# Kernel optimization log

Hardware: AMD Instinct MI355X
Metric: run time of the kernel (lower is better)

The kernel has to match this reference:

```python
import jax, jax.numpy as jnp
import numpy as np

# Mamba2 hyperparameters (from init_kwargs + mamba_ssm defaults)
D_MODEL = 1024
D_STATE = 64
D_CONV = 4
EXPAND = 2
HEADDIM = 64                      # mamba_ssm default
D_INNER = EXPAND * D_MODEL        # 2048
NHEADS = D_INNER // HEADDIM       # 32
NGROUPS = 1
CONV_DIM = D_INNER + 2 * NGROUPS * D_STATE      # 2176
D_IN_PROJ = 2 * D_INNER + 2 * NGROUPS * D_STATE + NHEADS  # 4256
BATCH, SEQLEN = 4, 2048


def setup_inputs() -> dict:
    key = jax.random.key(0)
    ks = jax.random.split(key, 8)
    x = jax.random.normal(ks[0], (BATCH, SEQLEN, D_MODEL), dtype=jnp.float32)
    W_in = jax.random.normal(ks[1], (D_MODEL, D_IN_PROJ), dtype=jnp.float32) * 0.02
    conv_w = jax.random.normal(ks[2], (CONV_DIM, D_CONV), dtype=jnp.float32) * 0.2
    conv_b = jnp.zeros((CONV_DIM,), dtype=jnp.float32)
    # dt_bias = inverse-softplus of dt ~ U(1e-3, 0.1), as in mamba_ssm init
    dt = jnp.exp(jax.random.uniform(ks[3], (NHEADS,)) * (np.log(0.1) - np.log(1e-3)) + np.log(1e-3))
    dt_bias = dt + jnp.log(-jnp.expm1(-dt))
    A_log = jnp.log(jax.random.uniform(ks[4], (NHEADS,), minval=1.0, maxval=16.0))
    D = jnp.ones((NHEADS,), dtype=jnp.float32)
    norm_w = jnp.ones((D_INNER,), dtype=jnp.float32)
    W_out = jax.random.normal(ks[5], (D_INNER, D_MODEL), dtype=jnp.float32) * 0.02
    return {"x": x, "W_in": W_in, "conv_w": conv_w, "conv_b": conv_b,
            "dt_bias": dt_bias, "A_log": A_log, "D": D, "norm_w": norm_w, "W_out": W_out}


def _mamba2_forward(x, W_in, conv_w, conv_b, dt_bias, A_log, D, norm_w, W_out):
    Bsz, L, _ = x.shape
    zxbcdt = x @ W_in                                   # [B, L, D_IN_PROJ]
    z = zxbcdt[..., :D_INNER]                           # gate
    xBC = zxbcdt[..., D_INNER:D_INNER + CONV_DIM]
    dt = zxbcdt[..., D_INNER + CONV_DIM:]               # [B, L, H]
    dt = jax.nn.softplus(dt + dt_bias)

    # causal depthwise conv1d over time, kernel width D_CONV
    xp = jnp.pad(xBC, ((0, 0), (D_CONV - 1, 0), (0, 0)))
    xc = sum(xp[:, k:k + L, :] * conv_w[:, k] for k in range(D_CONV))
    xBC = jax.nn.silu(xc + conv_b)

    xh = xBC[..., :D_INNER].reshape(Bsz, L, NHEADS, HEADDIM)   # [B,L,H,P]
    Bm = xBC[..., D_INNER:D_INNER + D_STATE]                   # [B,L,N] (ngroups=1)
    Cm = xBC[..., D_INNER + D_STATE:]                          # [B,L,N]
    A = -jnp.exp(A_log)                                        # [H]

    # selective SSM scan: h_t = h_{t-1}*exp(dt_t*A) + dt_t * x_t (outer) B_t ; y_t = C_t . h_t
    def step(h, inp):
        dt_t, x_t, B_t, C_t = inp                 # [B,H],[B,H,P],[B,N],[B,N]
        dA = jnp.exp(dt_t * A)                    # [B,H]
        h = h * dA[..., None, None] + (dt_t[..., None] * x_t)[..., None] * B_t[:, None, None, :]
        y_t = jnp.einsum('bhpn,bn->bhp', h, C_t)
        return h, y_t

    h0 = jnp.zeros((Bsz, NHEADS, HEADDIM, D_STATE), dtype=x.dtype)
    inputs = (jnp.moveaxis(dt, 1, 0), jnp.moveaxis(xh, 1, 0),
              jnp.moveaxis(Bm, 1, 0), jnp.moveaxis(Cm, 1, 0))
    _, ys = jax.lax.scan(step, h0, inputs)                     # [L,B,H,P]
    y = jnp.moveaxis(ys, 0, 1) + xh * D[None, None, :, None]   # skip term D*x
    y = y.reshape(Bsz, L, D_INNER)

    # gated RMSNorm: norm(y * silu(z)) * weight
    y = y * jax.nn.silu(z)
    y = y * jax.lax.rsqrt(jnp.mean(y * y, axis=-1, keepdims=True) + 1e-5) * norm_w
    return y @ W_out


def reference(x, W_in, conv_w, conv_b, dt_bias, A_log, D, norm_w, W_out):
    return _mamba2_forward(x, W_in, conv_w, conv_b, dt_bias, A_log, D, norm_w, W_out)
```

## Files before the change

kernel.cpp:

```cpp
#include <hip/hip_runtime.h>
#include <hip/hip_bf16.h>

#define B_SZ   4
#define SEQ    2048
#define DM     1024
#define DIN    2048
#define DST    64
#define NH     32
#define HD     64
#define CONVD  2176
#define DPROJ  4256
#define NPAD1  4352
#define MROWS  (B_SZ*SEQ)
#define QC     64
#define NC     (SEQ/QC)

typedef __attribute__((ext_vector_type(8))) __bf16 bf16x8;
typedef __attribute__((ext_vector_type(4))) __bf16 bf16x4;
typedef __attribute__((ext_vector_type(4))) float  floatx4;

__device__ __forceinline__ int swz(int row, int col) {
    return row * 64 + ((((col >> 3) ^ (row & 7)) << 3) | (col & 7));
}
__device__ __forceinline__ float bfbits2f(unsigned short u) {
    return __uint_as_float(((unsigned int)u) << 16);
}
__device__ __forceinline__ unsigned short f2bfbits(float f) {
    union { __bf16 h; unsigned short u; } cv; cv.h = (__bf16)f; return cv.u;
}

__global__ __launch_bounds__(256) void dtw_prep_kernel(const float* __restrict__ W_in,
                                                       float* __restrict__ dtWc) {
    int idx = blockIdx.x * 256 + threadIdx.x;
    int k = idx >> 5, h = idx & 31;
    dtWc[idx] = W_in[(size_t)k * DPROJ + 2 * DIN + 2 * DST + h];
}

__global__ __launch_bounds__(256) void cvt_dt_kernel(const float* __restrict__ x,
                                                     const float* __restrict__ dtWc,
                                                     __bf16* __restrict__ xbf,
                                                     float* __restrict__ dtraw) {
    __shared__ float xs[4][DM];
    __shared__ float red[4][8][32];
    const int row0 = blockIdx.x * 4;
    const int tid = threadIdx.x;
    #pragma unroll
    for (int r = 0; r < 4; r++) {
        float4 v = ((const float4*)(x + (size_t)(row0 + r) * DM))[tid];
        bf16x4 o;
        o[0] = (__bf16)v.x; o[1] = (__bf16)v.y; o[2] = (__bf16)v.z; o[3] = (__bf16)v.w;
        *(bf16x4*)(xbf + (size_t)(row0 + r) * DM + tid * 4) = o;
        xs[r][tid * 4 + 0] = v.x; xs[r][tid * 4 + 1] = v.y;
        xs[r][tid * 4 + 2] = v.z; xs[r][tid * 4 + 3] = v.w;
    }
    __syncthreads();
    const int part = tid >> 5, h = tid & 31;
    const float* wb = dtWc + part * 128 * 32 + h;
    const int kb = part * 128;
    float s0 = 0.f, s1 = 0.f, s2 = 0.f, s3 = 0.f;
    for (int j = 0; j < 128; j++) {
        float w = wb[j * 32];
        s0 = fmaf(xs[0][kb + j], w, s0);
        s1 = fmaf(xs[1][kb + j], w, s1);
        s2 = fmaf(xs[2][kb + j], w, s2);
        s3 = fmaf(xs[3][kb + j], w, s3);
    }
    red[0][part][h] = s0; red[1][part][h] = s1;
    red[2][part][h] = s2; red[3][part][h] = s3;
    __syncthreads();
    if (tid < 128) {
        int r = tid >> 5, hh = tid & 31;
        float s = 0.f;
        #pragma unroll
        for (int p = 0; p < 8; p++) s += red[r][p][hh];
        dtraw[(size_t)(row0 + r) * NH + hh] = s;
    }
}

__global__ __launch_bounds__(256) void transpose_cvt_kernel(const float* __restrict__ src,
                                                            __bf16* __restrict__ dst,
                                                            int R, int C, int Crows) {
    __shared__ float tile[32][33];
    int r0 = blockIdx.x * 32, c0 = blockIdx.y * 32;
    int tx = threadIdx.x & 31, ty = threadIdx.x >> 5;
    #pragma unroll
    for (int i = 0; i < 4; i++) {
        int r = r0 + ty + i * 8, c = c0 + tx;
        float v = (r < R && c < C) ? src[(size_t)r * C + c] : 0.f;
        tile[ty + i * 8][tx] = v;
    }
    __syncthreads();
    #pragma unroll
    for (int i = 0; i < 4; i++) {
        int cc = c0 + ty + i * 8, rr = r0 + tx;
        if (cc < Crows && rr < R)
            dst[(size_t)cc * R + rr] = (__bf16)tile[tx][ty + i * 8];
    }
}

template<int STORE_BF16>
__global__ __launch_bounds__(256) void gemm_bt_kernel(const __bf16* __restrict__ A,
                                                      const __bf16* __restrict__ Bt,
                                                      float* __restrict__ Cf,
                                                      __bf16* __restrict__ Cb,
                                                      int M, int N, int K) {
    __shared__ __align__(16) __bf16 As[128][32];
    __shared__ __align__(16) __bf16 Bs[128][32];
    const int tid = threadIdx.x;
    const int m0 = blockIdx.x * 128, n0 = blockIdx.y * 128;
    const int wave = tid >> 6, lane = tid & 63;
    const int wm = (wave & 1) << 6, wn = (wave >> 1) << 6;
    const int lm = lane & 15, lq = lane >> 4;

    floatx4 acc[4][4] = {};

    for (int k0 = 0; k0 < K; k0 += 32) {
        #pragma unroll
        for (int r = 0; r < 2; r++) {
            int c = tid + (r << 8);
            int row = c >> 2, off = (c & 3) << 3;
            __builtin_amdgcn_global_load_lds(
                reinterpret_cast<const unsigned int*>(&A[(size_t)(m0 + row) * K + k0 + off]),
                reinterpret_cast<unsigned int*>(&As[0][0] + (size_t)c * 8), 16, 0, 0);
            __builtin_amdgcn_global_load_lds(
                reinterpret_cast<const unsigned int*>(&Bt[(size_t)(n0 + row) * K + k0 + off]),
                reinterpret_cast<unsigned int*>(&Bs[0][0] + (size_t)c * 8), 16, 0, 0);
        }
        __syncthreads();
        bf16x8 af[4], bfr[4];
        #pragma unroll
        for (int i = 0; i < 4; i++)
            af[i] = *(const bf16x8*)(&As[wm + i * 16 + lm][lq * 8]);
        #pragma unroll
        for (int i = 0; i < 4; i++)
            bfr[i] = *(const bf16x8*)(&Bs[wn + i * 16 + lm][lq * 8]);
        #pragma unroll
        for (int mi = 0; mi < 4; mi++)
            #pragma unroll
            for (int ni = 0; ni < 4; ni++)
                acc[mi][ni] = __builtin_amdgcn_mfma_f32_16x16x32_bf16(af[mi], bfr[ni], acc[mi][ni], 0, 0, 0);
        __syncthreads();
    }

    #pragma unroll
    for (int mi = 0; mi < 4; mi++) {
        #pragma unroll
        for (int r = 0; r < 4; r++) {
            int row = m0 + wm + mi * 16 + lq * 4 + r;
            #pragma unroll
            for (int ni = 0; ni < 4; ni++) {
                int col = n0 + wn + ni * 16 + lm;
                if (col < N) {
                    if (STORE_BF16) Cb[(size_t)row * N + col] = (__bf16)acc[mi][ni][r];
                    else            Cf[(size_t)row * N + col] = acc[mi][ni][r];
                }
            }
        }
    }
}

__global__ __launch_bounds__(256) void conv_silu_kernel(const __bf16* __restrict__ zx,
                                                        const float* __restrict__ cw,
                                                        const float* __restrict__ cb,
                                                        __bf16* __restrict__ out) {
    int c = blockIdx.x * 256 + threadIdx.x;
    if (c >= CONVD) return;
    int g = blockIdx.y;
    int b = g >> 9;
    int t0 = (g & 511) << 2;
    const __bf16* base = zx + ((size_t)b * SEQ) * DPROJ + DIN + c;
    float xbuf[7];
    #pragma unroll
    for (int i = 0; i < 7; i++) {
        int tt = t0 + i - 3;
        xbuf[i] = (tt >= 0) ? (float)base[(size_t)tt * DPROJ] : 0.f;
    }
    float w0 = cw[c * 4 + 0], w1 = cw[c * 4 + 1], w2 = cw[c * 4 + 2], w3 = cw[c * 4 + 3];
    float bias = cb[c];
    __bf16* orow = out + ((size_t)b * SEQ + t0) * CONVD + c;
    #pragma unroll
    for (int s = 0; s < 4; s++) {
        float v = bias + w0 * xbuf[s] + w1 * xbuf[s + 1] + w2 * xbuf[s + 2] + w3 * xbuf[s + 3];
        orow[(size_t)s * CONVD] = (__bf16)(v / (1.f + __expf(-v)));
    }
}

__global__ __launch_bounds__(256) void dt_prep_kernel(const float* __restrict__ dtraw,
                                                      const float* __restrict__ dt_bias,
                                                      const float* __restrict__ A_log,
                                                      float* __restrict__ dtv,
                                                      float* __restrict__ cum) {
    int blk = blockIdx.x;
    int b = blk >> 5, h = blk & 31;
    int wave = threadIdx.x >> 6, lane = threadIdx.x & 63;
    float Ah = -__expf(A_log[h]);
    float dtb = dt_bias[h];
    for (int c = wave; c < NC; c += 4) {
        int t = c * QC + lane;
        float u = dtraw[((size_t)b * SEQ + t) * NH + h] + dtb;
        float d = fmaxf(u, 0.f) + log1pf(__expf(-fabsf(u)));
        float s = d * Ah;
        #pragma unroll
        for (int o = 1; o < 64; o <<= 1) {
            float v = __shfl_up(s, o);
            if (lane >= o) s += v;
        }
        size_t idx = (size_t)blk * SEQ + t;
        dtv[idx] = d;
        cum[idx] = s;
    }
}

__global__ __launch_bounds__(256) void chunk_state_kernel(const __bf16* __restrict__ xc,
                                                          const float* __restrict__ dtv,
                                                          const float* __restrict__ cum,
                                                          __bf16* __restrict__ Sbuf) {
    const int blk = blockIdx.x;
    const int hq = blk & 7;
    const int bc = blk >> 3;
    const int c = bc & (NC - 1), b = bc >> 5;
    const int tid = threadIdx.x;
    const int wave = tid >> 6, lane = tid & 63;
    const int lm = lane & 15, q = lane >> 4;
    const int h = hq * 4 + wave;

    __shared__ __align__(16) __bf16 sBt[4096];
    __shared__ __align__(16) __bf16 sXw[4][4096];

    const size_t rowbase = (size_t)b * SEQ + (size_t)c * QC;
    {
        int k = tid & 31, n0 = (tid >> 5) * 8;
        unsigned short u0[8], u1[8];
        *(uint4*)u0 = *(const uint4*)(xc + (rowbase + 2 * k) * CONVD + DIN + n0);
        *(uint4*)u1 = *(const uint4*)(xc + (rowbase + 2 * k + 1) * CONVD + DIN + n0);
        #pragma unroll
        for (int i = 0; i < 8; i++) {
            unsigned int v = (unsigned int)u0[i] | ((unsigned int)u1[i] << 16);
            ((unsigned int*)sBt)[swz(n0 + i, 2 * k) >> 1] = v;
        }
    }
    const float* cump = cum + (size_t)(b * NH + h) * SEQ + (size_t)c * QC;
    const float* dtp  = dtv + (size_t)(b * NH + h) * SEQ + (size_t)c * QC;
    {
        int k = lane & 31, ph = (lane >> 5) * 32;
        float clast = cump[63];
        float w0 = dtp[2 * k]     * __expf(clast - cump[2 * k]);
        float w1 = dtp[2 * k + 1] * __expf(clast - cump[2 * k + 1]);
        unsigned short u0[32], u1[32];
        const __bf16* r0 = xc + (rowbase + 2 * k) * CONVD + h * 64 + ph;
        const __bf16* r1 = xc + (rowbase + 2 * k + 1) * CONVD + h * 64 + ph;
        #pragma unroll
        for (int i = 0; i < 4; i++) {
            ((uint4*)u0)[i] = ((const uint4*)r0)[i];
            ((uint4*)u1)[i] = ((const uint4*)r1)[i];
        }
        unsigned int* dstw = (unsigned int*)sXw[wave];
        #pragma unroll
        for (int i = 0; i < 32; i++) {
            unsigned int lo = f2bfbits(bfbits2f(u0[i]) * w0);
            unsigned int hi = f2bfbits(bfbits2f(u1[i]) * w1);
            dstw[swz(ph + i, 2 * k) >> 1] = lo | (hi << 16);
        }
    }
    __syncthreads();

    floatx4 acc[4][4] = {};
    #pragma unroll
    for (int kb = 0; kb < 2; kb++) {
        bf16x8 aX[4], bB[4];
        #pragma unroll
        for (int pi = 0; pi < 4; pi++)
            aX[pi] = *(const bf16x8*)(&sXw[wave][swz(pi * 16 + lm, kb * 32 + q * 8)]);
        #pragma unroll
        for (int ni = 0; ni < 4; ni++)
            bB[ni] = *(const bf16x8*)(&sBt[swz(ni * 16 + lm, kb * 32 + q * 8)]);
        #pragma unroll
        for (int pi = 0; pi < 4; pi++)
            #pragma unroll
            for (int ni = 0; ni < 4; ni++)
                acc[pi][ni] = __builtin_amdgcn_mfma_f32_16x16x32_bf16(aX[pi], bB[ni], acc[pi][ni], 0, 0, 0);
    }
    __bf16* Sp = Sbuf + ((size_t)(b * NC + c) * NH + h) * (HD * DST);
    #pragma unroll
    for (int pi = 0; pi < 4; pi++)
        #pragma unroll
        for (int r = 0; r < 4; r++) {
            int p = pi * 16 + q * 4 + r;
            #pragma unroll
            for (int ni = 0; ni < 4; ni++)
                Sp[p * 64 + ni * 16 + lm] = (__bf16)acc[pi][ni][r];
        }
}

__global__ __launch_bounds__(256) void state_scan_kernel(__bf16* __restrict__ Sbuf,
                                                         const float* __restrict__ cum) {
    int blk = blockIdx.x;
    int b = blk >> 5, h = blk & 31;
    int off = threadIdx.x * 16;
    float run[16];
    #pragma unroll
    for (int n = 0; n < 16; n++) run[n] = 0.f;
    for (int c = 0; c < NC; c++) {
        __bf16* Sp = Sbuf + ((size_t)(b * NC + c) * NH + h) * (HD * DST) + off;
        float tmp[16];
        #pragma unroll
        for (int n = 0; n < 16; n++) tmp[n] = (float)Sp[n];
        #pragma unroll
        for (int n = 0; n < 16; n++) Sp[n] = (__bf16)run[n];
        float P = __expf(cum[(size_t)blk * SEQ + c * QC + QC - 1]);
        #pragma unroll
        for (int n = 0; n < 16; n++) run[n] = fmaf(run[n], P, tmp[n]);
    }
}

__global__ __launch_bounds__(128) void chunk_out_kernel(const __bf16* __restrict__ xc,
                                                        const float* __restrict__ dtv,
                                                        const float* __restrict__ cum,
                                                        const __bf16* __restrict__ Sbuf,
                                                        const float* __restrict__ Dv,
                                                        __bf16* __restrict__ y) {
    const int blk = blockIdx.x;
    const int hp = blk & 15;
    const int bc = blk >> 4;
    const int c = bc & (NC - 1), b = bc >> 5;
    const int tid = threadIdx.x;
    const int wave = tid >> 6, lane = tid & 63;
    const int lm = lane & 15, q = lane >> 4;
    const int h = hp * 2 + wave;

    __shared__ __align__(16) __bf16 sC[4096];
    __shared__ __align__(16) __bf16 sB[4096];
    __shared__ __align__(16) __bf16 sXt[2][4096];
    __shared__ __align__(16) __bf16 sP[2][4096];

    const size_t rowbase = (size_t)b * SEQ + (size_t)c * QC;
    {
        int r = tid >> 1, c0 = (tid & 1) * 32;
        const __bf16* gB = xc + (rowbase + r) * CONVD + DIN + c0;
        const __bf16* gC = xc + (rowbase + r) * CONVD + DIN + DST + c0;
        #pragma unroll
        for (int i = 0; i < 4; i++) {
            *(uint4*)(&sB[swz(r, c0 + i * 8)]) = *(const uint4*)(gB + i * 8);
            *(uint4*)(&sC[swz(r, c0 + i * 8)]) = *(const uint4*)(gC + i * 8);
        }
    }
    {
        int k = lane & 31, ph = (lane >> 5) * 32;
        unsigned short u0[32], u1[32];
        const __bf16* r0 = xc + (rowbase + 2 * k) * CONVD + h * 64 + ph;
        const __bf16* r1 = xc + (rowbase + 2 * k + 1) * CONVD + h * 64 + ph;
        #pragma unroll
        for (int i = 0; i < 4; i++) {
            ((uint4*)u0)[i] = ((const uint4*)r0)[i];
            ((uint4*)u1)[i] = ((const uint4*)r1)[i];
        }
        unsigned int* dstw = (unsigned int*)sXt[wave];
        #pragma unroll
        for (int i = 0; i < 32; i++)
            dstw[swz(ph + i, 2 * k) >> 1] = (unsigned int)u0[i] | ((unsigned int)u1[i] << 16);
    }
    __syncthreads();

    const float* cump = cum + (size_t)(b * NH + h) * SEQ + (size_t)c * QC;
    const float* dtp  = dtv + (size_t)(b * NH + h) * SEQ + (size_t)c * QC;
    float cumv = cump[lane], dtvv = dtp[lane];
    float ct[4][4];
    #pragma unroll
    for (int ti = 0; ti < 4; ti++)
        #pragma unroll
        for (int r = 0; r < 4; r++)
            ct[ti][r] = __shfl(cumv, ti * 16 + q * 4 + r);
    float cums_l[4], dtv_l[4];
    #pragma unroll
    for (int si = 0; si < 4; si++) {
        cums_l[si] = __shfl(cumv, si * 16 + lm);
        dtv_l[si]  = __shfl(dtvv, si * 16 + lm);
    }

    bf16x8 afC[4][2];
    #pragma unroll
    for (int ti = 0; ti < 4; ti++)
        #pragma unroll
        for (int kb = 0; kb < 2; kb++)
            afC[ti][kb] = *(const bf16x8*)(&sC[swz(ti * 16 + lm, kb * 32 + q * 8)]);

    floatx4 accG[4][4] = {};
    #pragma unroll
    for (int kb = 0; kb < 2; kb++) {
        bf16x8 bfB[4];
        #pragma unroll
        for (int si = 0; si < 4; si++)
            bfB[si] = *(const bf16x8*)(&sB[swz(si * 16 + lm, kb * 32 + q * 8)]);
        #pragma unroll
        for (int ti = 0; ti < 4; ti++)
            #pragma unroll
            for (int si = 0; si < 4; si++)
                if (si <= ti)
                    accG[ti][si] = __builtin_amdgcn_mfma_f32_16x16x32_bf16(afC[ti][kb], bfB[si], accG[ti][si], 0, 0, 0);
    }

    __bf16* P = sP[wave];
    #pragma unroll
    for (int ti = 0; ti < 4; ti++)
        #pragma unroll
        for (int si = 0; si < 4; si++) {
            if (si > ti) continue;
            #pragma unroll
            for (int r = 0; r < 4; r++) {
                int t = ti * 16 + q * 4 + r;
                float arg = fminf(ct[ti][r] - cums_l[si], 0.f);
                float val = dtv_l[si] * __expf(arg) * accG[ti][si][r];
                if (ti == si && lm > q * 4 + r) val = 0.f;
                P[swz(t, si * 16 + lm)] = (__bf16)val;
            }
        }
    #pragma unroll
    for (int r = 0; r < 4; r++) {
        P[swz(q * 4 + r, 16 + lm)] = (__bf16)0.f;
        P[swz(32 + q * 4 + r, 48 + lm)] = (__bf16)0.f;
    }

    floatx4 accY[4][4] = {};
    const __bf16* Sp = Sbuf + ((size_t)(b * NC + c) * NH + h) * (HD * DST);
    #pragma unroll
    for (int kb = 0; kb < 2; kb++) {
        bf16x8 bS[4];
        #pragma unroll
        for (int pi = 0; pi < 4; pi++)
            bS[pi] = *(const bf16x8*)(Sp + (pi * 16 + lm) * 64 + kb * 32 + q * 8);
        #pragma unroll
        for (int ti = 0; ti < 4; ti++)
            #pragma unroll
            for (int pi = 0; pi < 4; pi++)
                accY[ti][pi] = __builtin_amdgcn_mfma_f32_16x16x32_bf16(afC[ti][kb], bS[pi], accY[ti][pi], 0, 0, 0);
    }
    float ert[4][4];
    #pragma unroll
    for (int ti = 0; ti < 4; ti++)
        #pragma unroll
        for (int r = 0; r < 4; r++)
            ert[ti][r] = __expf(ct[ti][r]);
    #pragma unroll
    for (int ti = 0; ti < 4; ti++)
        #pragma unroll
        for (int pi = 0; pi < 4; pi++)
            #pragma unroll
            for (int r = 0; r < 4; r++)
                accY[ti][pi][r] *= ert[ti][r];

    #pragma unroll
    for (int kb = 0; kb < 2; kb++) {
        bf16x8 bX[4];
        #pragma unroll
        for (int pi = 0; pi < 4; pi++)
            bX[pi] = *(const bf16x8*)(&sXt[wave][swz(pi * 16 + lm, kb * 32 + q * 8)]);
        #pragma unroll
        for (int ti = 0; ti < 4; ti++) {
            if (ti < 2 * kb) continue;
            bf16x8 aP = *(const bf16x8*)(&sP[wave][swz(ti * 16 + lm, kb * 32 + q * 8)]);
            #pragma unroll
            for (int pi = 0; pi < 4; pi++)
                accY[ti][pi] = __builtin_amdgcn_mfma_f32_16x16x32_bf16(aP, bX[pi], accY[ti][pi], 0, 0, 0);
        }
    }

    float Dh = Dv[h];
    #pragma unroll
    for (int ti = 0; ti < 4; ti++)
        #pragma unroll
        for (int r = 0; r < 4; r++) {
            int t = ti * 16 + q * 4 + r;
            __bf16* yrow = y + (rowbase + t) * DIN + h * 64;
            #pragma unroll
            for (int pi = 0; pi < 4; pi++) {
                int p = pi * 16 + lm;
                float xv = (float)sXt[wave][swz(p, t)];
                yrow[p] = (__bf16)(accY[ti][pi][r] + Dh * xv);
            }
        }
}

__global__ __launch_bounds__(256) void gate_norm_kernel(__bf16* __restrict__ y,
                                                        const __bf16* __restrict__ zx,
                                                        const float* __restrict__ nw) {
    int row = blockIdx.x;
    int tid = threadIdx.x;
    __bf16* yr = y + (size_t)row * DIN;
    const __bf16* zr = zx + (size_t)row * DPROJ;
    float v[8]; float ss = 0.f;
    #pragma unroll
    for (int i = 0; i < 8; i++) {
        int c = i * 256 + tid;
        float z = (float)zr[c];
        float val = (float)yr[c] * (z / (1.f + __expf(-z)));
        v[i] = val; ss += val * val;
    }
    __shared__ float red[4];
    int lane = tid & 63, wave = tid >> 6;
    for (int o = 32; o > 0; o >>= 1) ss += __shfl_down(ss, o);
    if (lane == 0) red[wave] = ss;
    __syncthreads();
    float tot = red[0] + red[1] + red[2] + red[3];
    float scale = rsqrtf(tot * (1.f / (float)DIN) + 1e-5f);
    #pragma unroll
    for (int i = 0; i < 8; i++) {
        int c = i * 256 + tid;
        yr[c] = (__bf16)(v[i] * scale * nw[c]);
    }
}

extern "C" void kernel_launch(void* const* d_in, const int* in_sizes, int n_in,
                              void* d_out, int out_size, void* d_ws, size_t ws_size,
                              hipStream_t stream) {
    const float* x       = (const float*)d_in[0];
    const float* W_in    = (const float*)d_in[1];
    const float* conv_w  = (const float*)d_in[2];
    const float* conv_b  = (const float*)d_in[3];
    const float* dt_bias = (const float*)d_in[4];
    const float* A_log   = (const float*)d_in[5];
    const float* Dv      = (const float*)d_in[6];
    const float* norm_w  = (const float*)d_in[7];
    const float* W_out   = (const float*)d_in[8];
    float* out = (float*)d_out;

    char* ws = (char*)d_ws;
    size_t off = 0;
    auto take = [&](size_t bytes) { void* p = ws + off; off = (off + bytes + 255) & ~(size_t)255; return p; };
    __bf16* xbf    = (__bf16*)take((size_t)MROWS * DM * 2);
    __bf16* WinT   = (__bf16*)take((size_t)NPAD1 * DM * 2);
    __bf16* WoutT  = (__bf16*)take((size_t)DM * DIN * 2);
    __bf16* zx     = (__bf16*)take((size_t)MROWS * DPROJ * 2);
    __bf16* xc     = (__bf16*)take((size_t)MROWS * CONVD * 2);
    __bf16* yf     = (__bf16*)take((size_t)MROWS * DIN * 2);
    float*  dtraw  = (float*) take((size_t)MROWS * NH * 4);
    float*  dtv    = (float*) take((size_t)B_SZ * NH * SEQ * 4);
    float*  cum    = (float*) take((size_t)B_SZ * NH * SEQ * 4);
    __bf16* Sbuf   = (__bf16*)take((size_t)B_SZ * NC * NH * HD * DST * 2);
    float*  dtWc   = (float*) take((size_t)DM * NH * 4);
    (void)ws_size;

    dtw_prep_kernel<<<dim3(DM * NH / 256), 256, 0, stream>>>(W_in, dtWc);
    cvt_dt_kernel<<<dim3(MROWS / 4), 256, 0, stream>>>(x, dtWc, xbf, dtraw);
    transpose_cvt_kernel<<<dim3(DM / 32, NPAD1 / 32), 256, 0, stream>>>(W_in, WinT, DM, DPROJ, NPAD1);
    transpose_cvt_kernel<<<dim3(DIN / 32, DM / 32), 256, 0, stream>>>(W_out, WoutT, DIN, DM, DM);
    gemm_bt_kernel<1><<<dim3(MROWS / 128, (DPROJ + 127) / 128), 256, 0, stream>>>(
        xbf, WinT, nullptr, zx, MROWS, DPROJ, DM);
    conv_silu_kernel<<<dim3((CONVD + 255) / 256, B_SZ * SEQ / 4), 256, 0, stream>>>(zx, conv_w, conv_b, xc);
    dt_prep_kernel<<<dim3(B_SZ * NH), 256, 0, stream>>>(dtraw, dt_bias, A_log, dtv, cum);
    chunk_state_kernel<<<dim3(B_SZ * NC * (NH / 4)), 256, 0, stream>>>(xc, dtv, cum, Sbuf);
    state_scan_kernel<<<dim3(B_SZ * NH), 256, 0, stream>>>(Sbuf, cum);
    chunk_out_kernel<<<dim3(B_SZ * NC * (NH / 2)), 128, 0, stream>>>(xc, dtv, cum, Sbuf, Dv, yf);
    gate_norm_kernel<<<dim3(MROWS), 256, 0, stream>>>(yf, zx, norm_w);
    gemm_bt_kernel<0><<<dim3(MROWS / 128, DM / 128), 256, 0, stream>>>(
        yf, WoutT, out, nullptr, MROWS, DM, DIN);
}
```

Baseline: 399.3 us.

## Reorder GEMM LDS layout, vectorize conv and norm, fold D skip into P

```diff
diff --git a/kernel.cpp b/kernel.cpp
--- a/kernel.cpp
+++ b/kernel.cpp
@@ -104,12 +104,11 @@
                                                       float* __restrict__ Cf,
                                                       __bf16* __restrict__ Cb,
                                                       int M, int N, int K) {
-    __shared__ __align__(16) __bf16 As[128][32];
-    __shared__ __align__(16) __bf16 Bs[128][32];
+    __shared__ __align__(16) __bf16 As[4096];
+    __shared__ __align__(16) __bf16 Bs[4096];
     const int tid = threadIdx.x;
     const int m0 = blockIdx.x * 128, n0 = blockIdx.y * 128;
     const int wave = tid >> 6, lane = tid & 63;
-    const int wm = (wave & 1) << 6, wn = (wave >> 1) << 6;
     const int lm = lane & 15, lq = lane >> 4;
 
     floatx4 acc[4][4] = {};
@@ -118,22 +117,24 @@
         #pragma unroll
         for (int r = 0; r < 2; r++) {
             int c = tid + (r << 8);
-            int row = c >> 2, off = (c & 3) << 3;
+            int ln = c & 63;
+            int row = ((c >> 6) << 4) + (ln & 15);
+            int off = (ln >> 4) << 3;
             __builtin_amdgcn_global_load_lds(
                 reinterpret_cast<const unsigned int*>(&A[(size_t)(m0 + row) * K + k0 + off]),
-                reinterpret_cast<unsigned int*>(&As[0][0] + (size_t)c * 8), 16, 0, 0);
+                reinterpret_cast<unsigned int*>(As + (size_t)c * 8), 16, 0, 0);
             __builtin_amdgcn_global_load_lds(
                 reinterpret_cast<const unsigned int*>(&Bt[(size_t)(n0 + row) * K + k0 + off]),
-                reinterpret_cast<unsigned int*>(&Bs[0][0] + (size_t)c * 8), 16, 0, 0);
+                reinterpret_cast<unsigned int*>(Bs + (size_t)c * 8), 16, 0, 0);
         }
         __syncthreads();
         bf16x8 af[4], bfr[4];
         #pragma unroll
         for (int i = 0; i < 4; i++)
-            af[i] = *(const bf16x8*)(&As[wm + i * 16 + lm][lq * 8]);
+            af[i] = *(const bf16x8*)(As + ((((wave & 1) << 2) + i) << 9) + (lane << 3));
         #pragma unroll
         for (int i = 0; i < 4; i++)
-            bfr[i] = *(const bf16x8*)(&Bs[wn + i * 16 + lm][lq * 8]);
+            bfr[i] = *(const bf16x8*)(Bs + ((((wave >> 1) << 2) + i) << 9) + (lane << 3));
         #pragma unroll
         for (int mi = 0; mi < 4; mi++)
             #pragma unroll
@@ -142,6 +143,7 @@
         __syncthreads();
     }
 
+    const int wm = (wave & 1) << 6, wn = (wave >> 1) << 6;
     #pragma unroll
     for (int mi = 0; mi < 4; mi++) {
         #pragma unroll
@@ -163,25 +165,42 @@
                                                         const float* __restrict__ cw,
                                                         const float* __restrict__ cb,
                                                         __bf16* __restrict__ out) {
-    int c = blockIdx.x * 256 + threadIdx.x;
-    if (c >= CONVD) return;
-    int g = blockIdx.y;
-    int b = g >> 9;
-    int t0 = (g & 511) << 2;
-    const __bf16* base = zx + ((size_t)b * SEQ) * DPROJ + DIN + c;
-    float xbuf[7];
-    #pragma unroll
-    for (int i = 0; i < 7; i++) {
-        int tt = t0 + i - 3;
-        xbuf[i] = (tt >= 0) ? (float)base[(size_t)tt * DPROJ] : 0.f;
-    }
-    float w0 = cw[c * 4 + 0], w1 = cw[c * 4 + 1], w2 = cw[c * 4 + 2], w3 = cw[c * 4 + 3];
-    float bias = cb[c];
-    __bf16* orow = out + ((size_t)b * SEQ + t0) * CONVD + c;
-    #pragma unroll
-    for (int s = 0; s < 4; s++) {
-        float v = bias + w0 * xbuf[s] + w1 * xbuf[s + 1] + w2 * xbuf[s + 2] + w3 * xbuf[s + 3];
-        orow[(size_t)s * CONVD] = (__bf16)(v / (1.f + __expf(-v)));
+    const int tid = threadIdx.x;
+    const int tc = tid & 15, tt = tid >> 4;
+    const int c0 = (blockIdx.x * 16 + tc) * 8;
+    const int tg = blockIdx.y * 16 + tt;
+    const int b = tg >> 8, t0 = (tg & 255) << 3;
+
+    float xb[11][8];
+    #pragma unroll
+    for (int i = 0; i < 11; i++) {
+        int t = t0 + i - 3;
+        if (t >= 0) {
+            bf16x8 v = *(const bf16x8*)(zx + ((size_t)(b * SEQ + t)) * DPROJ + DIN + c0);
+            #pragma unroll
+            for (int j = 0; j < 8; j++) xb[i][j] = (float)v[j];
+        } else {
+            #pragma unroll
+            for (int j = 0; j < 8; j++) xb[i][j] = 0.f;
+        }
+    }
+    float w0[8], w1[8], w2[8], w3[8], bias[8];
+    #pragma unroll
+    for (int j = 0; j < 8; j++) {
+        float4 w = *(const float4*)(cw + (size_t)(c0 + j) * 4);
+        w0[j] = w.x; w1[j] = w.y; w2[j] = w.z; w3[j] = w.w;
+        bias[j] = cb[c0 + j];
+    }
+    #pragma unroll
+    for (int s = 0; s < 8; s++) {
+        bf16x8 o;
+        #pragma unroll
+        for (int j = 0; j < 8; j++) {
+            float v = bias[j] + w0[j] * xb[s][j] + w1[j] * xb[s + 1][j]
+                              + w2[j] * xb[s + 2][j] + w3[j] * xb[s + 3][j];
+            o[j] = (__bf16)(v / (1.f + __expf(-v)));
+        }
+        *(bf16x8*)(out + ((size_t)(b * SEQ + t0 + s)) * CONVD + c0) = o;
     }
 }
 
@@ -328,10 +347,11 @@
     const int lm = lane & 15, q = lane >> 4;
     const int h = hp * 2 + wave;
 
-    __shared__ __align__(16) __bf16 sC[4096];
-    __shared__ __align__(16) __bf16 sB[4096];
-    __shared__ __align__(16) __bf16 sXt[2][4096];
-    __shared__ __align__(16) __bf16 sP[2][4096];
+    __shared__ __align__(16) __bf16 smem[16384];
+    __bf16* sB  = smem;
+    __bf16* sC  = smem + 4096;
+    __bf16* sXt = smem + 8192 + (wave << 12);
+    __bf16* sP  = smem + (wave << 12);
 
     const size_t rowbase = (size_t)b * SEQ + (size_t)c * QC;
     {
@@ -354,7 +374,7 @@
             ((uint4*)u0)[i] = ((const uint4*)r0)[i];
             ((uint4*)u1)[i] = ((const uint4*)r1)[i];
         }
-        unsigned int* dstw = (unsigned int*)sXt[wave];
+        unsigned int* dstw = (unsigned int*)sXt;
         #pragma unroll
         for (int i = 0; i < 32; i++)
             dstw[swz(ph + i, 2 * k) >> 1] = (unsigned int)u0[i] | ((unsigned int)u1[i] << 16);
@@ -398,8 +418,9 @@
                 if (si <= ti)
                     accG[ti][si] = __builtin_amdgcn_mfma_f32_16x16x32_bf16(afC[ti][kb], bfB[si], accG[ti][si], 0, 0, 0);
     }
-
-    __bf16* P = sP[wave];
+    __syncthreads();
+
+    float Dh = Dv[h];
     #pragma unroll
     for (int ti = 0; ti < 4; ti++)
         #pragma unroll
@@ -410,15 +431,19 @@
                 int t = ti * 16 + q * 4 + r;
                 float arg = fminf(ct[ti][r] - cums_l[si], 0.f);
                 float val = dtv_l[si] * __expf(arg) * accG[ti][si][r];
-                if (ti == si && lm > q * 4 + r) val = 0.f;
-                P[swz(t, si * 16 + lm)] = (__bf16)val;
+                if (ti == si) {
+                    if (lm > q * 4 + r) val = 0.f;
+                    else if (lm == q * 4 + r) val += Dh;
+                }
+                sP[swz(t, si * 16 + lm)] = (__bf16)val;
             }
         }
     #pragma unroll
     for (int r = 0; r < 4; r++) {
-        P[swz(q * 4 + r, 16 + lm)] = (__bf16)0.f;
-        P[swz(32 + q * 4 + r, 48 + lm)] = (__bf16)0.f;
-    }
+        sP[swz(q * 4 + r, 16 + lm)] = (__bf16)0.f;
+        sP[swz(32 + q * 4 + r, 48 + lm)] = (__bf16)0.f;
+    }
+    __syncthreads();
 
     floatx4 accY[4][4] = {};
     const __bf16* Sp = Sbuf + ((size_t)(b * NC + c) * NH + h) * (HD * DST);
@@ -434,37 +459,32 @@
             for (int pi = 0; pi < 4; pi++)
                 accY[ti][pi] = __builtin_amdgcn_mfma_f32_16x16x32_bf16(afC[ti][kb], bS[pi], accY[ti][pi], 0, 0, 0);
     }
-    float ert[4][4];
     #pragma unroll
     for (int ti = 0; ti < 4; ti++)
         #pragma unroll
-        for (int r = 0; r < 4; r++)
-            ert[ti][r] = __expf(ct[ti][r]);
-    #pragma unroll
-    for (int ti = 0; ti < 4; ti++)
-        #pragma unroll
-        for (int pi = 0; pi < 4; pi++)
-            #pragma unroll
-            for (int r = 0; r < 4; r++)
-                accY[ti][pi][r] *= ert[ti][r];
+        for (int r = 0; r < 4; r++) {
+            float e = __expf(ct[ti][r]);
+            #pragma unroll
+            for (int pi = 0; pi < 4; pi++)
+                accY[ti][pi][r] *= e;
+        }
 
     #pragma unroll
     for (int kb = 0; kb < 2; kb++) {
         bf16x8 bX[4];
         #pragma unroll
         for (int pi = 0; pi < 4; pi++)
-            bX[pi] = *(const bf16x8*)(&sXt[wave][swz(pi * 16 + lm, kb * 32 + q * 8)]);
+            bX[pi] = *(const bf16x8*)(&sXt[swz(pi * 16 + lm, kb * 32 + q * 8)]);
         #pragma unroll
         for (int ti = 0; ti < 4; ti++) {
             if (ti < 2 * kb) continue;
-            bf16x8 aP = *(const bf16x8*)(&sP[wave][swz(ti * 16 + lm, kb * 32 + q * 8)]);
+            bf16x8 aP = *(const bf16x8*)(&sP[swz(ti * 16 + lm, kb * 32 + q * 8)]);
             #pragma unroll
             for (int pi = 0; pi < 4; pi++)
                 accY[ti][pi] = __builtin_amdgcn_mfma_f32_16x16x32_bf16(aP, bX[pi], accY[ti][pi], 0, 0, 0);
         }
     }
 
-    float Dh = Dv[h];
     #pragma unroll
     for (int ti = 0; ti < 4; ti++)
         #pragma unroll
@@ -472,11 +492,8 @@
             int t = ti * 16 + q * 4 + r;
             __bf16* yrow = y + (rowbase + t) * DIN + h * 64;
             #pragma unroll
-            for (int pi = 0; pi < 4; pi++) {
-                int p = pi * 16 + lm;
-                float xv = (float)sXt[wave][swz(p, t)];
-                yrow[p] = (__bf16)(accY[ti][pi][r] + Dh * xv);
-            }
+            for (int pi = 0; pi < 4; pi++)
+                yrow[pi * 16 + lm] = (__bf16)accY[ti][pi][r];
         }
 }
 
@@ -485,15 +502,16 @@
                                                         const float* __restrict__ nw) {
     int row = blockIdx.x;
     int tid = threadIdx.x;
-    __bf16* yr = y + (size_t)row * DIN;
-    const __bf16* zr = zx + (size_t)row * DPROJ;
+    __bf16* yr = y + (size_t)row * DIN + tid * 8;
+    const __bf16* zr = zx + (size_t)row * DPROJ + tid * 8;
+    bf16x8 yv = *(const bf16x8*)yr;
+    bf16x8 zv = *(const bf16x8*)zr;
     float v[8]; float ss = 0.f;
     #pragma unroll
-    for (int i = 0; i < 8; i++) {
-        int c = i * 256 + tid;
-        float z = (float)zr[c];
-        float val = (float)yr[c] * (z / (1.f + __expf(-z)));
-        v[i] = val; ss += val * val;
+    for (int j = 0; j < 8; j++) {
+        float z = (float)zv[j];
+        float val = (float)yv[j] * (z / (1.f + __expf(-z)));
+        v[j] = val; ss += val * val;
     }
     __shared__ float red[4];
     int lane = tid & 63, wave = tid >> 6;
@@ -502,11 +520,11 @@
     __syncthreads();
     float tot = red[0] + red[1] + red[2] + red[3];
     float scale = rsqrtf(tot * (1.f / (float)DIN) + 1e-5f);
-    #pragma unroll
-    for (int i = 0; i < 8; i++) {
-        int c = i * 256 + tid;
-        yr[c] = (__bf16)(v[i] * scale * nw[c]);
-    }
+    const float* nwp = nw + tid * 8;
+    bf16x8 o;
+    #pragma unroll
+    for (int j = 0; j < 8; j++) o[j] = (__bf16)(v[j] * scale * nwp[j]);
+    *(bf16x8*)yr = o;
 }
 
 extern "C" void kernel_launch(void* const* d_in, const int* in_sizes, int n_in,
@@ -545,7 +563,7 @@
     transpose_cvt_kernel<<<dim3(DIN / 32, DM / 32), 256, 0, stream>>>(W_out, WoutT, DIN, DM, DM);
     gemm_bt_kernel<1><<<dim3(MROWS / 128, (DPROJ + 127) / 128), 256, 0, stream>>>(
         xbf, WinT, nullptr, zx, MROWS, DPROJ, DM);
-    conv_silu_kernel<<<dim3((CONVD + 255) / 256, B_SZ * SEQ / 4), 256, 0, stream>>>(zx, conv_w, conv_b, xc);
+    conv_silu_kernel<<<dim3(17, 64), 256, 0, stream>>>(zx, conv_w, conv_b, xc);
     dt_prep_kernel<<<dim3(B_SZ * NH), 256, 0, stream>>>(dtraw, dt_bias, A_log, dtv, cum);
     chunk_state_kernel<<<dim3(B_SZ * NC * (NH / 4)), 256, 0, stream>>>(xc, dtv, cum, Sbuf);
     state_scan_kernel<<<dim3(B_SZ * NH), 256, 0, stream>>>(Sbuf, cum);
```

New measurement: 449.8 us. +12.6%, slower.
